# Kernel tuning notes

Measured on AMD Instinct MI355X. Metric: run time of the kernel, lower is better.

Reference implementation:

```python
import jax, jax.numpy as jnp
from jax import lax
import numpy as np

D_MODEL = 512
D_STATE = 16
D_CONV = 4
D_INNER = 1024  # expand=2
DT_RANK = 32    # ceil(512/16)
N_LAYERS = 2
IN_DIM = 1024
N_CLS = 2
N_INST = 4096


def setup_inputs() -> dict:
    key = jax.random.key(0)
    ks = jax.random.split(key, 16)
    g = lambda i, shape, s=0.02: jax.random.normal(ks[i], shape, jnp.float32) * s
    x = jax.random.normal(ks[0], (1, N_INST, IN_DIM), jnp.float32)
    inp = {
        'x': x,
        'fc1_w': g(1, (D_MODEL, IN_DIM)),
        'fc1_b': jnp.zeros((D_MODEL,), jnp.float32),
        'ln_w': jnp.ones((N_LAYERS, D_MODEL), jnp.float32),
        'ln_b': jnp.zeros((N_LAYERS, D_MODEL), jnp.float32),
        'in_proj_w': g(2, (N_LAYERS, 2 * D_INNER, D_MODEL)),
        'conv_w': g(3, (N_LAYERS, D_INNER, 1, D_CONV), 0.1),
        'conv_b': jnp.zeros((N_LAYERS, D_INNER), jnp.float32),
        'x_proj_w': g(4, (N_LAYERS, DT_RANK + 2 * D_STATE, D_INNER)),
        'dt_w': g(5, (N_LAYERS, D_INNER, DT_RANK), 0.1),
        'dt_b': jnp.full((N_LAYERS, D_INNER), -4.6, jnp.float32),  # softplus ~ 0.01
        'A_log': jnp.tile(jnp.log(jnp.arange(1, D_STATE + 1, dtype=jnp.float32))[None, None, :], (N_LAYERS, D_INNER, 1)),
        'D_p': jnp.ones((N_LAYERS, D_INNER), jnp.float32),
        'out_proj_w': g(6, (N_LAYERS, D_MODEL, D_INNER)),
        'norm_w': jnp.ones((D_MODEL,), jnp.float32),
        'norm_b': jnp.zeros((D_MODEL,), jnp.float32),
        'attn_w1': g(7, (128, D_MODEL)),
        'attn_b1': jnp.zeros((128,), jnp.float32),
        'attn_w2': g(8, (1, 128)),
        'attn_b2': jnp.zeros((1,), jnp.float32),
        'cls_w': g(9, (N_CLS, D_MODEL)),
        'cls_b': jnp.zeros((N_CLS,), jnp.float32),
    }
    return inp


def _layernorm(x, w, b, eps=1e-5):
    m = x.mean(-1, keepdims=True)
    v = ((x - m) ** 2).mean(-1, keepdims=True)
    return (x - m) * lax.rsqrt(v + eps) * w + b


def _mamba_block(u, in_w, cw, cb, xpw, dtw, dtb, A_log, D_p, ow):
    # u: (L, D_MODEL)
    xz = u @ in_w.T                       # (L, 2*D_INNER)
    xi, z = jnp.split(xz, 2, axis=-1)
    # causal depthwise conv1d over sequence
    xc = lax.conv_general_dilated(
        xi.T[None], cw, window_strides=(1,), padding=[(D_CONV - 1, 0)],
        dimension_numbers=('NCH', 'OIH', 'NCH'), feature_group_count=D_INNER,
    )[0].T + cb                           # (L, D_INNER)
    xc = jax.nn.silu(xc)
    dbc = xc @ xpw.T                      # (L, DT_RANK + 2*D_STATE)
    dt = jax.nn.softplus(dbc[:, :DT_RANK] @ dtw.T + dtb)          # (L, D_INNER)
    B = dbc[:, DT_RANK:DT_RANK + D_STATE]                          # (L, D_STATE)
    C = dbc[:, DT_RANK + D_STATE:]                                 # (L, D_STATE)
    A = -jnp.exp(A_log)                                            # (D_INNER, D_STATE)
    dA = jnp.exp(jnp.einsum('ld,dn->ldn', dt, A))                  # (L, D_INNER, D_STATE)
    dBx = jnp.einsum('ln,ld->ldn', B, dt * xc)                     # (L, D_INNER, D_STATE)

    def step(h, inp):
        dA_t, dBx_t, C_t = inp
        h = dA_t * h + dBx_t              # (D_INNER, D_STATE)
        return h, h @ C_t                 # y_t: (D_INNER,)

    _, ys = lax.scan(step, jnp.zeros((D_INNER, D_STATE), u.dtype), (dA, dBx, C))
    y = ys + D_p * xc
    y = y * jax.nn.silu(z)
    return y @ ow.T                       # (L, D_MODEL)


def reference(x, fc1_w, fc1_b, ln_w, ln_b, in_proj_w, conv_w, conv_b, x_proj_w,
              dt_w, dt_b, A_log, D_p, out_proj_w, norm_w, norm_b,
              attn_w1, attn_b1, attn_w2, attn_b2, cls_w, cls_b):
    h = jax.nn.relu(x[0] @ fc1_w.T + fc1_b)          # (N, 512); batch is 1
    for i in range(N_LAYERS):
        res = h
        hn = _layernorm(h, ln_w[i], ln_b[i])
        h = _mamba_block(hn, in_proj_w[i], conv_w[i], conv_b[i], x_proj_w[i],
                         dt_w[i], dt_b[i], A_log[i], D_p[i], out_proj_w[i]) + res
    h = _layernorm(h, norm_w, norm_b)                # (N, 512)
    # gated attention pooling: linear-tanh-linear + softmax over instances
    a = jnp.tanh(h @ attn_w1.T + attn_b1) @ attn_w2.T + attn_b2   # (N, 1)
    w = jax.nn.softmax(a[:, 0])                       # (N,)
    pooled = w @ h                                    # (512,)
    logits = pooled @ cls_w.T + cls_b                 # (N_CLS,)
    return logits[None, :]                            # (1, N_CLS)
```

## Files before the change

kernel.cpp:

```cpp
#include <hip/hip_runtime.h>
#include <math.h>

#define L 4096
#define DM 512
#define DI 1024
#define DS 16
#define RNK 32
#define NC 64
#define CT 64
#define BD 64

typedef unsigned short u16;
typedef __attribute__((ext_vector_type(8))) short bfv8;
typedef __attribute__((ext_vector_type(4))) float f32x4;

__device__ __forceinline__ u16 f2bf(float f) {
  unsigned int u = __float_as_uint(f);
  u = (u + 0x7fff + ((u >> 16) & 1)) >> 16;
  return (u16)u;
}
__device__ __forceinline__ float bf2f(u16 h) {
  return __uint_as_float(((unsigned int)h) << 16);
}

__device__ __forceinline__ void gload16(const void* g, void* l) {
  __builtin_amdgcn_global_load_lds(
      (const __attribute__((address_space(1))) void*)g,
      (__attribute__((address_space(3))) void*)l, 16, 0, 0);
}

__global__ __launch_bounds__(256) void split_bf(
    const float* __restrict__ in, u16* __restrict__ hi, u16* __restrict__ lo,
    int n4) {
  int i = blockIdx.x * 256 + threadIdx.x;
  if (i >= n4) return;
  float4 v = ((const float4*)in)[i];
  ushort4 h4, l4;
  h4.x = f2bf(v.x); l4.x = f2bf(v.x - bf2f(h4.x));
  h4.y = f2bf(v.y); l4.y = f2bf(v.y - bf2f(h4.y));
  h4.z = f2bf(v.z); l4.z = f2bf(v.z - bf2f(h4.z));
  h4.w = f2bf(v.w); l4.w = f2bf(v.w - bf2f(h4.w));
  ((ushort4*)hi)[i] = h4;
  ((ushort4*)lo)[i] = l4;
}

template <int BMT, int BN_, int WM, int WN, int ACT, int BIAS, int RES,
          int OSPLIT, int PARTIAL = 0>
__global__ __launch_bounds__(256) void gemm_mfma(
    const u16* __restrict__ Ah, const u16* __restrict__ Al,
    const u16* __restrict__ Wh, const u16* __restrict__ Wl,
    const float* __restrict__ bias, const float* __restrict__ res,
    float* __restrict__ Cf, u16* __restrict__ Ch, u16* __restrict__ Cl,
    int M, int N, int K) {
  constexpr int BK_ = 32;
  constexpr int MSUB = BMT / WM, NSUB = BN_ / WN;
  constexpr int MR = MSUB / 16, NR = NSUB / 16;
  __shared__ u16 smem[2 * BMT * BK_ + 2 * BN_ * BK_];
  u16* sAh = smem;
  u16* sAl = smem + BMT * BK_;
  u16* sBh = smem + 2 * BMT * BK_;
  u16* sBl = sBh + BN_ * BK_;
  const int lane = threadIdx.x & 63, wid = threadIdx.x >> 6;
  const int wrow = wid / WN, wcol = wid % WN;
  const int bm = blockIdx.y * BMT, bn = blockIdx.x * BN_;
  const int fr = lane & 15, kq = lane >> 4;
  const int kz = blockIdx.z;
  const int kslice = K / gridDim.z;
  const int kbeg = kz * kslice, kend = kbeg + kslice;

  f32x4 acc[MR][NR];
#pragma unroll
  for (int m = 0; m < MR; ++m)
#pragma unroll
    for (int n = 0; n < NR; ++n) acc[m][n] = (f32x4){0.f, 0.f, 0.f, 0.f};

  for (int kt = kbeg; kt < kend; kt += BK_) {
#pragma unroll
    for (int s = wid; s < BMT / 16; s += 4) {
      int chunk = s * 64 + lane;
      int row = chunk >> 2, c4 = chunk & 3;
      size_t go = (size_t)(bm + row) * K + kt + c4 * 8;
      gload16(Ah + go, sAh + s * 512);
      gload16(Al + go, sAl + s * 512);
    }
#pragma unroll
    for (int s = wid; s < BN_ / 16; s += 4) {
      int chunk = s * 64 + lane;
      int row = chunk >> 2, c4 = chunk & 3;
      size_t go = (size_t)(bn + row) * K + kt + c4 * 8;
      gload16(Wh + go, sBh + s * 512);
      gload16(Wl + go, sBl + s * 512);
    }
    __syncthreads();

    bfv8 ah[MR], al[MR], bh[NR], bl[NR];
#pragma unroll
    for (int m = 0; m < MR; ++m) {
      int row = wrow * MSUB + m * 16 + fr;
      ah[m] = *(const bfv8*)(sAh + row * 32 + kq * 8);
      al[m] = *(const bfv8*)(sAl + row * 32 + kq * 8);
    }
#pragma unroll
    for (int n = 0; n < NR; ++n) {
      int row = wcol * NSUB + n * 16 + fr;
      bh[n] = *(const bfv8*)(sBh + row * 32 + kq * 8);
      bl[n] = *(const bfv8*)(sBl + row * 32 + kq * 8);
    }
#pragma unroll
    for (int m = 0; m < MR; ++m)
#pragma unroll
      for (int n = 0; n < NR; ++n) {
        acc[m][n] = __builtin_amdgcn_mfma_f32_16x16x32_bf16(ah[m], bh[n], acc[m][n], 0, 0, 0);
        acc[m][n] = __builtin_amdgcn_mfma_f32_16x16x32_bf16(ah[m], bl[n], acc[m][n], 0, 0, 0);
        acc[m][n] = __builtin_amdgcn_mfma_f32_16x16x32_bf16(al[m], bh[n], acc[m][n], 0, 0, 0);
      }
    __syncthreads();
  }

#pragma unroll
  for (int m = 0; m < MR; ++m)
#pragma unroll
    for (int n = 0; n < NR; ++n) {
      int col = bn + wcol * NSUB + n * 16 + fr;
      float bv = 0.f;
      if (BIAS) bv = bias[col];
#pragma unroll
      for (int j = 0; j < 4; ++j) {
        int row = bm + wrow * MSUB + m * 16 + kq * 4 + j;
        if (PARTIAL) {
          Cf[(size_t)kz * M * N + (size_t)row * N + col] = acc[m][n][j];
          continue;
        }
        float v = acc[m][n][j] + bv;
        if (ACT == 1) v = fmaxf(v, 0.f);
        if (ACT == 2) v = tanhf(v);
        if (RES) v += res[(size_t)row * N + col];
        if (OSPLIT) {
          u16 hv = f2bf(v);
          Ch[(size_t)row * N + col] = hv;
          Cl[(size_t)row * N + col] = f2bf(v - bf2f(hv));
        } else {
          Cf[(size_t)row * N + col] = v;
        }
      }
    }
}

template <int KS, int ACT, int BIAS, int RES>
__global__ __launch_bounds__(256) void kreduce(
    const float* __restrict__ part, const float* __restrict__ bias,
    const float* __restrict__ res, float* __restrict__ Cf, int MN, int N) {
  int i = blockIdx.x * 256 + threadIdx.x;
  if (i * 4 >= MN) return;
  const float4* p4 = (const float4*)part;
  float4 s = p4[i];
#pragma unroll
  for (int k = 1; k < KS; ++k) {
    float4 v = p4[i + (size_t)k * (MN / 4)];
    s.x += v.x; s.y += v.y; s.z += v.z; s.w += v.w;
  }
  if (BIAS) {
    int col = (i * 4) % N;
    float4 b = *(const float4*)(bias + col);
    s.x += b.x; s.y += b.y; s.z += b.z; s.w += b.w;
  }
  if (ACT == 1) {
    s.x = fmaxf(s.x, 0.f); s.y = fmaxf(s.y, 0.f);
    s.z = fmaxf(s.z, 0.f); s.w = fmaxf(s.w, 0.f);
  }
  if (ACT == 2) {
    s.x = tanhf(s.x); s.y = tanhf(s.y); s.z = tanhf(s.z); s.w = tanhf(s.w);
  }
  if (RES) {
    float4 r = ((const float4*)res)[i];
    s.x += r.x; s.y += r.y; s.z += r.z; s.w += r.w;
  }
  ((float4*)Cf)[i] = s;
}

template <int F32OUT>
__global__ __launch_bounds__(64) void ln_kernel(
    const float* __restrict__ x, const float* __restrict__ w,
    const float* __restrict__ b, float* __restrict__ of,
    u16* __restrict__ oh, u16* __restrict__ ol) {
  const int l = blockIdx.x, t = threadIdx.x;
  const float* row = x + (size_t)l * DM;
  float4 v0 = *(const float4*)(row + t * 8);
  float4 v1 = *(const float4*)(row + t * 8 + 4);
  float vals[8] = {v0.x, v0.y, v0.z, v0.w, v1.x, v1.y, v1.z, v1.w};
  float s = 0.f;
#pragma unroll
  for (int i = 0; i < 8; ++i) s += vals[i];
#pragma unroll
  for (int off = 1; off < 64; off <<= 1) s += __shfl_xor(s, off);
  float m = s * (1.f / DM);
  float q = 0.f;
#pragma unroll
  for (int i = 0; i < 8; ++i) { float dd = vals[i] - m; q += dd * dd; }
#pragma unroll
  for (int off = 1; off < 64; off <<= 1) q += __shfl_xor(q, off);
  float rs = 1.f / sqrtf(q * (1.f / DM) + 1e-5f);
  float4 w0 = *(const float4*)(w + t * 8);
  float4 w1 = *(const float4*)(w + t * 8 + 4);
  float4 b0 = *(const float4*)(b + t * 8);
  float4 b1 = *(const float4*)(b + t * 8 + 4);
  float wv[8] = {w0.x, w0.y, w0.z, w0.w, w1.x, w1.y, w1.z, w1.w};
  float bb[8] = {b0.x, b0.y, b0.z, b0.w, b1.x, b1.y, b1.z, b1.w};
  ushort4 h4[2], l4[2];
#pragma unroll
  for (int i = 0; i < 8; ++i) {
    float o = (vals[i] - m) * rs * wv[i] + bb[i];
    u16 hv = f2bf(o);
    ((u16*)h4)[i] = hv;
    ((u16*)l4)[i] = f2bf(o - bf2f(hv));
    vals[i] = o;
  }
  size_t base = (size_t)l * DM + t * 8;
  *(ushort4*)(oh + base) = h4[0];
  *(ushort4*)(oh + base + 4) = h4[1];
  *(ushort4*)(ol + base) = l4[0];
  *(ushort4*)(ol + base + 4) = l4[1];
  if (F32OUT) {
    *(float4*)(of + base) = make_float4(vals[0], vals[1], vals[2], vals[3]);
    *(float4*)(of + base + 4) = make_float4(vals[4], vals[5], vals[6], vals[7]);
  }
}

__global__ __launch_bounds__(256) void conv_silu(
    const u16* __restrict__ xzh, const u16* __restrict__ xzl,
    const float* __restrict__ cw, const float* __restrict__ cb,
    u16* __restrict__ xch, u16* __restrict__ xcl) {
  const int idx = blockIdx.x * 256 + threadIdx.x;
  const int l = idx >> 10, d = idx & 1023;
  float s = cb[d];
  float4 w4 = *(const float4*)(cw + d * 4);
  const float wk[4] = {w4.x, w4.y, w4.z, w4.w};
#pragma unroll
  for (int k = 0; k < 4; ++k) {
    int ll = l - 3 + k;
    if (ll >= 0) {
      size_t o = (size_t)ll * (2 * DI) + d;
      s += (bf2f(xzh[o]) + bf2f(xzl[o])) * wk[k];
    }
  }
  float v = s / (1.f + __expf(-s));
  u16 hv = f2bf(v);
  xch[idx] = hv;
  xcl[idx] = f2bf(v - bf2f(hv));
}

__global__ __launch_bounds__(256) void dt_fast(
    const float* __restrict__ dbc, const float* __restrict__ dtw,
    const float* __restrict__ dtb, float* __restrict__ dt) {
  __shared__ float s[32][33];
  const int t = threadIdx.x;
  const int d = blockIdx.x * 256 + t;
  const int l0 = blockIdx.y * 32;
  {
    int r = t >> 3, c4 = t & 7;
    float4 v = *(const float4*)(dbc + (size_t)(l0 + r) * 64 + c4 * 4);
    s[r][c4 * 4 + 0] = v.x; s[r][c4 * 4 + 1] = v.y;
    s[r][c4 * 4 + 2] = v.z; s[r][c4 * 4 + 3] = v.w;
  }
  __syncthreads();
  float wk[RNK];
#pragma unroll
  for (int k = 0; k < RNK; k += 4) {
    float4 w4 = *(const float4*)(dtw + (size_t)d * RNK + k);
    wk[k] = w4.x; wk[k + 1] = w4.y; wk[k + 2] = w4.z; wk[k + 3] = w4.w;
  }
  const float bias = dtb[d];
  for (int l = 0; l < 32; ++l) {
    float acc = bias;
#pragma unroll
    for (int k = 0; k < RNK; ++k) acc += s[l][k] * wk[k];
    float sp = fmaxf(acc, 0.f) + __logf(1.f + __expf(-fabsf(acc)));
    dt[(size_t)(l0 + l) * DI + d] = sp;
  }
}

__global__ __launch_bounds__(256) void scan_part1(
    const u16* __restrict__ xch, const u16* __restrict__ xcl,
    const float* __restrict__ dt, const float* __restrict__ dbc,
    const float* __restrict__ A_log, float* __restrict__ Pbuf,
    float* __restrict__ Sbuf) {
  __shared__ float sdt[CT * BD];
  __shared__ float sx[CT * BD];
  __shared__ float sB[CT * 16];
  const int t = threadIdx.x;
  const int d0 = blockIdx.x * BD;
  const int c = blockIdx.y;
  const int l0 = c * CT;
#pragma unroll
  for (int it = 0; it < 16; ++it) {
    int idx = it * 256 + t;
    int l = idx >> 6, dc = idx & 63;
    size_t o = (size_t)(l0 + l) * DI + d0 + dc;
    sdt[idx] = dt[o];
    sx[idx] = bf2f(xch[o]) + bf2f(xcl[o]);
  }
#pragma unroll
  for (int it = 0; it < 4; ++it) {
    int idx = it * 256 + t;
    int l = idx >> 4, col = idx & 15;
    sB[idx] = dbc[(size_t)(l0 + l) * 64 + RNK + col];
  }
  __syncthreads();
  const int sub = t & 3;
  const int dl = t >> 2;
  const int d = d0 + dl;
  float A[4];
  {
    float4 a4 = *(const float4*)(A_log + (size_t)d * DS + sub * 4);
    A[0] = -__expf(a4.x); A[1] = -__expf(a4.y);
    A[2] = -__expf(a4.z); A[3] = -__expf(a4.w);
  }
  float S4[4] = {0.f, 0.f, 0.f, 0.f};
  float dtsum = 0.f;
  for (int l = 0; l < CT; ++l) {
    float dtv = sdt[l * BD + dl];
    float xv = sx[l * BD + dl];
    float4 Bv = *(const float4*)(sB + l * 16 + sub * 4);
    float dx = dtv * xv;
    dtsum += dtv;
    const float B[4] = {Bv.x, Bv.y, Bv.z, Bv.w};
#pragma unroll
    for (int j = 0; j < 4; ++j) {
      float dA = __expf(dtv * A[j]);
      S4[j] = dA * S4[j] + B[j] * dx;
    }
  }
  size_t po = ((size_t)c * DI + d) * DS + sub * 4;
  *(float4*)(Pbuf + po) = make_float4(__expf(A[0] * dtsum), __expf(A[1] * dtsum),
                                      __expf(A[2] * dtsum), __expf(A[3] * dtsum));
  *(float4*)(Sbuf + po) = make_float4(S4[0], S4[1], S4[2], S4[3]);
}

__global__ __launch_bounds__(256) void scan_carry(
    const float* __restrict__ Pbuf, float* __restrict__ Sbuf) {
  const int p = blockIdx.x * 256 + threadIdx.x;
  float H = 0.f;
  for (int c = 0; c < NC; ++c) {
    const size_t o = (size_t)c * (DI * DS) + p;
    float Pv = Pbuf[o], Sv = Sbuf[o];
    Sbuf[o] = H;
    H = Pv * H + Sv;
  }
}

__global__ __launch_bounds__(256) void scan_part2(
    const u16* __restrict__ xch, const u16* __restrict__ xcl,
    const float* __restrict__ dt, const float* __restrict__ dbc,
    const float* __restrict__ Hin, const u16* __restrict__ xzh,
    const u16* __restrict__ xzl, u16* __restrict__ yh, u16* __restrict__ yl,
    const float* __restrict__ A_log, const float* __restrict__ D_p) {
  __shared__ float sdt[CT * BD];
  __shared__ float sx[CT * BD];
  __shared__ float sB[CT * 16];
  __shared__ float sC[CT * 16];
  const int t = threadIdx.x;
  const int d0 = blockIdx.x * BD;
  const int c = blockIdx.y;
  const int l0 = c * CT;
#pragma unroll
  for (int it = 0; it < 16; ++it) {
    int idx = it * 256 + t;
    int l = idx >> 6, dc = idx & 63;
    size_t o = (size_t)(l0 + l) * DI + d0 + dc;
    sdt[idx] = dt[o];
    sx[idx] = bf2f(xch[o]) + bf2f(xcl[o]);
  }
#pragma unroll
  for (int it = 0; it < 4; ++it) {
    int idx = it * 256 + t;
    int l = idx >> 4, col = idx & 15;
    size_t ro = (size_t)(l0 + l) * 64 + RNK + col;
    sB[idx] = dbc[ro];
    sC[idx] = dbc[ro + DS];
  }
  __syncthreads();
  const int sub = t & 3;
  const int dl = t >> 2;
  const int d = d0 + dl;
  float A[4], hst[4];
  {
    float4 a4 = *(const float4*)(A_log + (size_t)d * DS + sub * 4);
    A[0] = -__expf(a4.x); A[1] = -__expf(a4.y);
    A[2] = -__expf(a4.z); A[3] = -__expf(a4.w);
    float4 h4 = *(const float4*)(Hin + ((size_t)c * DI + d) * DS + sub * 4);
    hst[0] = h4.x; hst[1] = h4.y; hst[2] = h4.z; hst[3] = h4.w;
  }
  const float Dp = D_p[d];
  for (int l = 0; l < CT; ++l) {
    float dtv = sdt[l * BD + dl];
    float xv = sx[l * BD + dl];
    float4 Bv = *(const float4*)(sB + l * 16 + sub * 4);
    float4 Cv = *(const float4*)(sC + l * 16 + sub * 4);
    float dx = dtv * xv;
    const float B[4] = {Bv.x, Bv.y, Bv.z, Bv.w};
    const float C[4] = {Cv.x, Cv.y, Cv.z, Cv.w};
    float y = 0.f;
#pragma unroll
    for (int j = 0; j < 4; ++j) {
      float dA = __expf(dtv * A[j]);
      hst[j] = dA * hst[j] + B[j] * dx;
      y += hst[j] * C[j];
    }
    y += __shfl_xor(y, 1);
    y += __shfl_xor(y, 2);
    if (sub == 0) {
      size_t o = (size_t)(l0 + l) * DI + d;
      size_t zo = (size_t)(l0 + l) * (2 * DI) + DI + d;
      float zv = bf2f(xzh[zo]) + bf2f(xzl[zo]);
      float yv = y + Dp * xv;
      float out = yv * (zv / (1.f + __expf(-zv)));
      u16 hv = f2bf(out);
      yh[o] = hv;
      yl[o] = f2bf(out - bf2f(hv));
    }
  }
}

__global__ __launch_bounds__(64) void attn2_kernel(
    const float* __restrict__ tb, const float* __restrict__ w2,
    const float* __restrict__ b2, float* __restrict__ avec) {
  const int l = blockIdx.x, t = threadIdx.x;
  float acc = tb[(size_t)l * 128 + t] * w2[t] +
              tb[(size_t)l * 128 + 64 + t] * w2[64 + t];
#pragma unroll
  for (int off = 1; off < 64; off <<= 1) acc += __shfl_xor(acc, off);
  if (t == 0) avec[l] = acc + b2[0];
}

__global__ __launch_bounds__(256) void softmax4096(
    const float* __restrict__ a, float* __restrict__ w) {
  __shared__ float sm[4];
  const int t = threadIdx.x;
  float vals[16];
  float m = -1e30f;
#pragma unroll
  for (int i = 0; i < 16; ++i) { vals[i] = a[t + i * 256]; m = fmaxf(m, vals[i]); }
#pragma unroll
  for (int off = 1; off < 64; off <<= 1) m = fmaxf(m, __shfl_xor(m, off));
  if ((t & 63) == 0) sm[t >> 6] = m;
  __syncthreads();
  m = fmaxf(fmaxf(sm[0], sm[1]), fmaxf(sm[2], sm[3]));
  __syncthreads();
  float s = 0.f;
#pragma unroll
  for (int i = 0; i < 16; ++i) { vals[i] = expf(vals[i] - m); s += vals[i]; }
#pragma unroll
  for (int off = 1; off < 64; off <<= 1) s += __shfl_xor(s, off);
  if ((t & 63) == 0) sm[t >> 6] = s;
  __syncthreads();
  s = sm[0] + sm[1] + sm[2] + sm[3];
  float inv = 1.f / s;
#pragma unroll
  for (int i = 0; i < 16; ++i) w[t + i * 256] = vals[i] * inv;
}

__global__ __launch_bounds__(256) void pooled_partial(
    const float* __restrict__ w, const float* __restrict__ hn,
    float* __restrict__ partial) {
  const int b = blockIdx.x;
  const int t = threadIdx.x;
  float acc0 = 0.f, acc1 = 0.f;
  for (int l = b * 128; l < b * 128 + 128; ++l) {
    float wl = w[l];
    acc0 += wl * hn[(size_t)l * DM + t];
    acc1 += wl * hn[(size_t)l * DM + t + 256];
  }
  partial[b * DM + t] = acc0;
  partial[b * DM + t + 256] = acc1;
}

__global__ __launch_bounds__(256) void pooled_reduce(
    const float* __restrict__ partial, float* __restrict__ pooled) {
  const int d = blockIdx.x * 256 + threadIdx.x;
  float s = 0.f;
  for (int b = 0; b < 32; ++b) s += partial[b * DM + d];
  pooled[d] = s;
}

__global__ __launch_bounds__(128) void logits_kernel(
    const float* __restrict__ pooled, const float* __restrict__ cls_w,
    const float* __restrict__ cls_b, float* __restrict__ out) {
  const int c = threadIdx.x >> 6, lane = threadIdx.x & 63;
  float acc = 0.f;
  for (int j = lane; j < DM; j += 64) acc += pooled[j] * cls_w[c * DM + j];
#pragma unroll
  for (int off = 1; off < 64; off <<= 1) acc += __shfl_xor(acc, off);
  if (lane == 0) out[c] = acc + cls_b[c];
}

extern "C" void kernel_launch(void* const* d_in, const int* in_sizes, int n_in,
                              void* d_out, int out_size, void* d_ws,
                              size_t ws_size, hipStream_t stream) {
  const float* x        = (const float*)d_in[0];
  const float* fc1_w    = (const float*)d_in[1];
  const float* fc1_b    = (const float*)d_in[2];
  const float* ln_w     = (const float*)d_in[3];
  const float* ln_b     = (const float*)d_in[4];
  const float* in_projw = (const float*)d_in[5];
  const float* conv_w   = (const float*)d_in[6];
  const float* conv_b   = (const float*)d_in[7];
  const float* x_projw  = (const float*)d_in[8];
  const float* dt_w     = (const float*)d_in[9];
  const float* dt_b     = (const float*)d_in[10];
  const float* A_log    = (const float*)d_in[11];
  const float* D_p      = (const float*)d_in[12];
  const float* out_projw= (const float*)d_in[13];
  const float* norm_w   = (const float*)d_in[14];
  const float* norm_b   = (const float*)d_in[15];
  const float* attn_w1  = (const float*)d_in[16];
  const float* attn_b1  = (const float*)d_in[17];
  const float* attn_w2  = (const float*)d_in[18];
  const float* attn_b2  = (const float*)d_in[19];
  const float* cls_w    = (const float*)d_in[20];
  const float* cls_b    = (const float*)d_in[21];

  char* p = (char*)d_ws;
  const size_t MB = 1024 * 1024;
  float* h    = (float*)(p);
  float* dbc  = (float*)(p + 8 * MB);
  float* dt   = (float*)(p + 9 * MB);
  float* tb   = dt;
  float* gpart= dt;
  float* Pbuf = (float*)(p + 25 * MB);
  float* Sbuf = (float*)(p + 29 * MB);
  float* xpart= Pbuf;
  float* hn   = Pbuf;
  float* avec = (float*)(p + 33 * MB);
  float* wvec = avec + L;
  float* part = wvec + L;
  float* pool = part + 32 * DM;
  u16* xzh = (u16*)(p + 34 * MB);
  u16* xzl = (u16*)(p + 50 * MB);
  float* apart = (float*)(p + 34 * MB);
  u16* yh  = (u16*)(p + 66 * MB);
  u16* yl  = (u16*)(p + 74 * MB);
  u16* hnh = yh;
  u16* hnl = yl;
  u16* xch = (u16*)(p + 82 * MB);
  u16* xcl = (u16*)(p + 90 * MB);
  u16* xh = xch;
  u16* xl = xcl;
  u16* wfh = (u16*)(p + 98 * MB);
  u16* wfl = wfh + 524288;
  u16* wih = (u16*)(p + 100 * MB);
  u16* wil = (u16*)(p + 104 * MB);
  u16* wxh = (u16*)(p + 108 * MB);
  u16* wxl = wxh + 131072;
  u16* woh = (u16*)(p + 109 * MB);
  u16* wol = (u16*)(p + 111 * MB);
  u16* wah = (u16*)(p + 113 * MB);
  u16* wal = wah + 65536;

  split_bf<<<4096, 256, 0, stream>>>(x, xh, xl, L * DI / 4);
  split_bf<<<512, 256, 0, stream>>>(fc1_w, wfh, wfl, 524288 / 4);
  split_bf<<<2048, 256, 0, stream>>>(in_projw, wih, wil, 2097152 / 4);
  split_bf<<<128, 256, 0, stream>>>(x_projw, wxh, wxl, 131072 / 4);
  split_bf<<<1024, 256, 0, stream>>>(out_projw, woh, wol, 1048576 / 4);
  split_bf<<<64, 256, 0, stream>>>(attn_w1, wah, wal, 65536 / 4);

  gemm_mfma<64, 128, 2, 2, 0, 0, 0, 0, 1><<<dim3(4, 64, 2), 256, 0, stream>>>(
      xh, xl, wfh, wfl, nullptr, nullptr, gpart, nullptr, nullptr,
      L, DM, 1024);
  kreduce<2, 1, 1, 0><<<2048, 256, 0, stream>>>(
      gpart, fc1_b, nullptr, h, L * DM, DM);

  for (int i = 0; i < 2; ++i) {
    ln_kernel<0><<<L, 64, 0, stream>>>(h, ln_w + i * DM, ln_b + i * DM,
                                       nullptr, hnh, hnl);
    gemm_mfma<64, 128, 2, 2, 0, 0, 0, 1><<<dim3(16, 64), 256, 0, stream>>>(
        hnh, hnl, wih + (size_t)i * 2 * DI * DM, wil + (size_t)i * 2 * DI * DM,
        nullptr, nullptr, nullptr, xzh, xzl, L, 2 * DI, DM);
    conv_silu<<<L * DI / 256, 256, 0, stream>>>(
        xzh, xzl, conv_w + (size_t)i * DI * 4, conv_b + (size_t)i * DI,
        xch, xcl);
    gemm_mfma<64, 64, 2, 2, 0, 0, 0, 0, 1><<<dim3(1, 64, 8), 256, 0, stream>>>(
        xch, xcl, wxh + (size_t)i * 64 * DI, wxl + (size_t)i * 64 * DI,
        nullptr, nullptr, xpart, nullptr, nullptr, L, 64, DI);
    kreduce<8, 0, 0, 0><<<256, 256, 0, stream>>>(
        xpart, nullptr, nullptr, dbc, L * 64, 64);
    dt_fast<<<dim3(DI / 256, L / 32), 256, 0, stream>>>(
        dbc, dt_w + (size_t)i * DI * RNK, dt_b + (size_t)i * DI, dt);
    scan_part1<<<dim3(DI / BD, NC), 256, 0, stream>>>(
        xch, xcl, dt, dbc, A_log + (size_t)i * DI * DS, Pbuf, Sbuf);
    scan_carry<<<DI * DS / 256, 256, 0, stream>>>(Pbuf, Sbuf);
    scan_part2<<<dim3(DI / BD, NC), 256, 0, stream>>>(
        xch, xcl, dt, dbc, Sbuf, xzh, xzl, yh, yl,
        A_log + (size_t)i * DI * DS, D_p + (size_t)i * DI);
    gemm_mfma<64, 128, 2, 2, 0, 0, 0, 0, 1><<<dim3(4, 64, 2), 256, 0, stream>>>(
        yh, yl, woh + (size_t)i * DM * DI, wol + (size_t)i * DM * DI,
        nullptr, nullptr, gpart, nullptr, nullptr, L, DM, DI);
    kreduce<2, 0, 0, 1><<<2048, 256, 0, stream>>>(
        gpart, nullptr, h, h, L * DM, DM);
  }

  ln_kernel<1><<<L, 64, 0, stream>>>(h, norm_w, norm_b, hn, hnh, hnl);
  gemm_mfma<64, 128, 2, 2, 0, 0, 0, 0, 1><<<dim3(1, 64, 4), 256, 0, stream>>>(
      hnh, hnl, wah, wal, nullptr, nullptr, apart, nullptr, nullptr,
      L, 128, DM);
  kreduce<4, 2, 1, 0><<<512, 256, 0, stream>>>(
      apart, attn_b1, nullptr, tb, L * 128, 128);
  attn2_kernel<<<L, 64, 0, stream>>>(tb, attn_w2, attn_b2, avec);
  softmax4096<<<1, 256, 0, stream>>>(avec, wvec);
  pooled_partial<<<32, 256, 0, stream>>>(wvec, hn, part);
  pooled_reduce<<<2, 256, 0, stream>>>(part, pool);
  logits_kernel<<<1, 128, 0, stream>>>(pool, cls_w, cls_b, (float*)d_out);
}
```

Measured before the change: 445.6 us.

## Fuse chunk-local scan output into part1; replace part2 recurrence with elementwise carry correction

The first scan pass now also computes the chunk-local output y (with zero initial state plus the D skip term) and stores the running cumulative dt per position. The second pass becomes a fully parallel elementwise kernel that adds the carried-in state contribution C·H·exp(A·cumdt) and applies the SiLU gate, so the sequential recurrence is no longer run twice. A small kernel precomputes -exp(A_log) once per layer. In exchange, the second pass now computes 16 exponentials per element and re-reads the y buffers. It also adds an extra rounding step because the local y is stored split into two bf16 halves.

```diff
diff --git a/kernel.cpp b/kernel.cpp
--- a/kernel.cpp
+++ b/kernel.cpp
@@ -279,14 +279,22 @@
   }
 }
 
-__global__ __launch_bounds__(256) void scan_part1(
+__global__ __launch_bounds__(256) void negexpA(
+    const float* __restrict__ A_log, float* __restrict__ negA, int n) {
+  int i = blockIdx.x * 256 + threadIdx.x;
+  if (i < n) negA[i] = -__expf(A_log[i]);
+}
+
+__global__ __launch_bounds__(256) void scan_fused1(
     const u16* __restrict__ xch, const u16* __restrict__ xcl,
-    const float* __restrict__ dt, const float* __restrict__ dbc,
-    const float* __restrict__ A_log, float* __restrict__ Pbuf,
-    float* __restrict__ Sbuf) {
+    float* __restrict__ dtg, const float* __restrict__ dbc,
+    const float* __restrict__ negA, u16* __restrict__ yh,
+    u16* __restrict__ yl, float* __restrict__ Pbuf, float* __restrict__ Sbuf,
+    const float* __restrict__ D_p) {
   __shared__ float sdt[CT * BD];
   __shared__ float sx[CT * BD];
   __shared__ float sB[CT * 16];
+  __shared__ float sC[CT * 16];
   const int t = threadIdx.x;
   const int d0 = blockIdx.x * BD;
   const int c = blockIdx.y;
@@ -296,14 +304,16 @@
     int idx = it * 256 + t;
     int l = idx >> 6, dc = idx & 63;
     size_t o = (size_t)(l0 + l) * DI + d0 + dc;
-    sdt[idx] = dt[o];
+    sdt[idx] = dtg[o];
     sx[idx] = bf2f(xch[o]) + bf2f(xcl[o]);
   }
 #pragma unroll
   for (int it = 0; it < 4; ++it) {
     int idx = it * 256 + t;
     int l = idx >> 4, col = idx & 15;
-    sB[idx] = dbc[(size_t)(l0 + l) * 64 + RNK + col];
+    size_t ro = (size_t)(l0 + l) * 64 + RNK + col;
+    sB[idx] = dbc[ro];
+    sC[idx] = dbc[ro + DS];
   }
   __syncthreads();
   const int sub = t & 3;
@@ -311,29 +321,43 @@
   const int d = d0 + dl;
   float A[4];
   {
-    float4 a4 = *(const float4*)(A_log + (size_t)d * DS + sub * 4);
-    A[0] = -__expf(a4.x); A[1] = -__expf(a4.y);
-    A[2] = -__expf(a4.z); A[3] = -__expf(a4.w);
-  }
-  float S4[4] = {0.f, 0.f, 0.f, 0.f};
-  float dtsum = 0.f;
+    float4 a4 = *(const float4*)(negA + (size_t)d * DS + sub * 4);
+    A[0] = a4.x; A[1] = a4.y; A[2] = a4.z; A[3] = a4.w;
+  }
+  float hst[4] = {0.f, 0.f, 0.f, 0.f};
+  const float Dp = D_p[d];
+  float csum = 0.f;
   for (int l = 0; l < CT; ++l) {
     float dtv = sdt[l * BD + dl];
     float xv = sx[l * BD + dl];
     float4 Bv = *(const float4*)(sB + l * 16 + sub * 4);
+    float4 Cv = *(const float4*)(sC + l * 16 + sub * 4);
     float dx = dtv * xv;
-    dtsum += dtv;
+    csum += dtv;
     const float B[4] = {Bv.x, Bv.y, Bv.z, Bv.w};
+    const float C[4] = {Cv.x, Cv.y, Cv.z, Cv.w};
+    float y = 0.f;
 #pragma unroll
     for (int j = 0; j < 4; ++j) {
       float dA = __expf(dtv * A[j]);
-      S4[j] = dA * S4[j] + B[j] * dx;
+      hst[j] = dA * hst[j] + B[j] * dx;
+      y += hst[j] * C[j];
+    }
+    y += __shfl_xor(y, 1);
+    y += __shfl_xor(y, 2);
+    if (sub == 0) {
+      size_t o = (size_t)(l0 + l) * DI + d;
+      float ypre = y + Dp * xv;
+      u16 hv = f2bf(ypre);
+      yh[o] = hv;
+      yl[o] = f2bf(ypre - bf2f(hv));
+      dtg[o] = csum;
     }
   }
   size_t po = ((size_t)c * DI + d) * DS + sub * 4;
-  *(float4*)(Pbuf + po) = make_float4(__expf(A[0] * dtsum), __expf(A[1] * dtsum),
-                                      __expf(A[2] * dtsum), __expf(A[3] * dtsum));
-  *(float4*)(Sbuf + po) = make_float4(S4[0], S4[1], S4[2], S4[3]);
+  *(float4*)(Pbuf + po) = make_float4(__expf(A[0] * csum), __expf(A[1] * csum),
+                                      __expf(A[2] * csum), __expf(A[3] * csum));
+  *(float4*)(Sbuf + po) = make_float4(hst[0], hst[1], hst[2], hst[3]);
 }
 
 __global__ __launch_bounds__(256) void scan_carry(
@@ -348,77 +372,36 @@
   }
 }
 
-__global__ __launch_bounds__(256) void scan_part2(
-    const u16* __restrict__ xch, const u16* __restrict__ xcl,
-    const float* __restrict__ dt, const float* __restrict__ dbc,
-    const float* __restrict__ Hin, const u16* __restrict__ xzh,
-    const u16* __restrict__ xzl, u16* __restrict__ yh, u16* __restrict__ yl,
-    const float* __restrict__ A_log, const float* __restrict__ D_p) {
-  __shared__ float sdt[CT * BD];
-  __shared__ float sx[CT * BD];
-  __shared__ float sB[CT * 16];
-  __shared__ float sC[CT * 16];
-  const int t = threadIdx.x;
-  const int d0 = blockIdx.x * BD;
-  const int c = blockIdx.y;
-  const int l0 = c * CT;
-#pragma unroll
-  for (int it = 0; it < 16; ++it) {
-    int idx = it * 256 + t;
-    int l = idx >> 6, dc = idx & 63;
-    size_t o = (size_t)(l0 + l) * DI + d0 + dc;
-    sdt[idx] = dt[o];
-    sx[idx] = bf2f(xch[o]) + bf2f(xcl[o]);
-  }
-#pragma unroll
-  for (int it = 0; it < 4; ++it) {
-    int idx = it * 256 + t;
-    int l = idx >> 4, col = idx & 15;
-    size_t ro = (size_t)(l0 + l) * 64 + RNK + col;
-    sB[idx] = dbc[ro];
-    sC[idx] = dbc[ro + DS];
-  }
-  __syncthreads();
-  const int sub = t & 3;
-  const int dl = t >> 2;
-  const int d = d0 + dl;
-  float A[4], hst[4];
-  {
-    float4 a4 = *(const float4*)(A_log + (size_t)d * DS + sub * 4);
-    A[0] = -__expf(a4.x); A[1] = -__expf(a4.y);
-    A[2] = -__expf(a4.z); A[3] = -__expf(a4.w);
-    float4 h4 = *(const float4*)(Hin + ((size_t)c * DI + d) * DS + sub * 4);
-    hst[0] = h4.x; hst[1] = h4.y; hst[2] = h4.z; hst[3] = h4.w;
-  }
-  const float Dp = D_p[d];
-  for (int l = 0; l < CT; ++l) {
-    float dtv = sdt[l * BD + dl];
-    float xv = sx[l * BD + dl];
-    float4 Bv = *(const float4*)(sB + l * 16 + sub * 4);
-    float4 Cv = *(const float4*)(sC + l * 16 + sub * 4);
-    float dx = dtv * xv;
-    const float B[4] = {Bv.x, Bv.y, Bv.z, Bv.w};
-    const float C[4] = {Cv.x, Cv.y, Cv.z, Cv.w};
-    float y = 0.f;
-#pragma unroll
-    for (int j = 0; j < 4; ++j) {
-      float dA = __expf(dtv * A[j]);
-      hst[j] = dA * hst[j] + B[j] * dx;
-      y += hst[j] * C[j];
-    }
-    y += __shfl_xor(y, 1);
-    y += __shfl_xor(y, 2);
-    if (sub == 0) {
-      size_t o = (size_t)(l0 + l) * DI + d;
-      size_t zo = (size_t)(l0 + l) * (2 * DI) + DI + d;
-      float zv = bf2f(xzh[zo]) + bf2f(xzl[zo]);
-      float yv = y + Dp * xv;
-      float out = yv * (zv / (1.f + __expf(-zv)));
-      u16 hv = f2bf(out);
-      yh[o] = hv;
-      yl[o] = f2bf(out - bf2f(hv));
-    }
-  }
+__global__ __launch_bounds__(256) void scan_part2elem(
+    const float* __restrict__ cumdt, const float* __restrict__ Hin,
+    const float* __restrict__ negA, const float* __restrict__ dbc,
+    const u16* __restrict__ xzh, const u16* __restrict__ xzl,
+    u16* __restrict__ yh, u16* __restrict__ yl) {
+  const int idx = blockIdx.x * 256 + threadIdx.x;
+  const int d = idx & (DI - 1), l = idx >> 10;
+  const int c = l >> 6;
+  const float cd = cumdt[idx];
+  const float* Hp = Hin + ((size_t)c * DI + d) * DS;
+  const float* Ap = negA + (size_t)d * DS;
+  const float* Cr = dbc + (size_t)l * 64 + RNK + DS;
+  float corr = 0.f;
+#pragma unroll
+  for (int n = 0; n < DS; n += 4) {
+    float4 a4 = *(const float4*)(Ap + n);
+    float4 h4 = *(const float4*)(Hp + n);
+    float4 c4 = *(const float4*)(Cr + n);
+    corr += c4.x * h4.x * __expf(a4.x * cd);
+    corr += c4.y * h4.y * __expf(a4.y * cd);
+    corr += c4.z * h4.z * __expf(a4.z * cd);
+    corr += c4.w * h4.w * __expf(a4.w * cd);
+  }
+  float y = bf2f(yh[idx]) + bf2f(yl[idx]) + corr;
+  size_t zo = (size_t)l * (2 * DI) + DI + d;
+  float zv = bf2f(xzh[zo]) + bf2f(xzl[zo]);
+  float out = y * (zv / (1.f + __expf(-zv)));
+  u16 hv = f2bf(out);
+  yh[idx] = hv;
+  yl[idx] = f2bf(out - bf2f(hv));
 }
 
 __global__ __launch_bounds__(64) void attn2_kernel(
@@ -534,6 +517,7 @@
   float* wvec = avec + L;
   float* part = wvec + L;
   float* pool = part + 32 * DM;
+  float* negA = (float*)(p + 33 * MB + 512 * 1024);
   u16* xzh = (u16*)(p + 34 * MB);
   u16* xzl = (u16*)(p + 50 * MB);
   float* apart = (float*)(p + 34 * MB);
@@ -585,12 +569,14 @@
         xpart, nullptr, nullptr, dbc, L * 64, 64);
     dt_fast<<<dim3(DI / 256, L / 32), 256, 0, stream>>>(
         dbc, dt_w + (size_t)i * DI * RNK, dt_b + (size_t)i * DI, dt);
-    scan_part1<<<dim3(DI / BD, NC), 256, 0, stream>>>(
-        xch, xcl, dt, dbc, A_log + (size_t)i * DI * DS, Pbuf, Sbuf);
+    negexpA<<<DI * DS / 256, 256, 0, stream>>>(
+        A_log + (size_t)i * DI * DS, negA, DI * DS);
+    scan_fused1<<<dim3(DI / BD, NC), 256, 0, stream>>>(
+        xch, xcl, dt, dbc, negA, yh, yl, Pbuf, Sbuf,
+        D_p + (size_t)i * DI);
     scan_carry<<<DI * DS / 256, 256, 0, stream>>>(Pbuf, Sbuf);
-    scan_part2<<<dim3(DI / BD, NC), 256, 0, stream>>>(
-        xch, xcl, dt, dbc, Sbuf, xzh, xzl, yh, yl,
-        A_log + (size_t)i * DI * DS, D_p + (size_t)i * DI);
+    scan_part2elem<<<L * DI / 256, 256, 0, stream>>>(
+        dt, Sbuf, negA, dbc, xzh, xzl, yh, yl);
     gemm_mfma<64, 128, 2, 2, 0, 0, 0, 0, 1><<<dim3(4, 64, 2), 256, 0, stream>>>(
         yh, yl, woh + (size_t)i * DM * DI, wol + (size_t)i * DM * DI,
         nullptr, nullptr, gpart, nullptr, nullptr, L, DM, DI);
```

New measurement: 464.6 us. +4.3%, slower.
